# Kernel tuning notes

Hardware: AMD Instinct MI355X
Metric: run time of the kernel (lower is better)

The kernel has to match this reference:

```python
import jax, jax.numpy as jnp
import numpy as np

D_MODEL, D_HEAD, N_HEAD, PERIOD = 1024, 64, 16, 30
B, T1, T2 = 2, 2048, 2048


def setup_inputs() -> dict:
    key = jax.random.key(0)
    ks = jax.random.split(key, 7)
    s_in = 1.0 / np.sqrt(D_MODEL)
    s_out = 1.0 / np.sqrt(N_HEAD * D_HEAD)
    return {
        "x": jax.random.normal(ks[0], (B, T1, D_MODEL), dtype=jnp.float32),
        "context": jax.random.normal(ks[1], (B, T2, D_MODEL), dtype=jnp.float32),
        "Wq": jax.random.uniform(ks[2], (N_HEAD * D_HEAD, D_MODEL), jnp.float32, -s_in, s_in),
        "Wk": jax.random.uniform(ks[3], (N_HEAD * D_HEAD, D_MODEL), jnp.float32, -s_in, s_in),
        "Wv": jax.random.uniform(ks[4], (N_HEAD * D_HEAD, D_MODEL), jnp.float32, -s_in, s_in),
        "Wo": jax.random.uniform(ks[5], (D_MODEL, N_HEAD * D_HEAD), jnp.float32, -s_out, s_out),
        "bo": jax.random.uniform(ks[6], (D_MODEL,), jnp.float32, -s_out, s_out),
    }


def reference(x, context, Wq, Wk, Wv, Wo, bo):
    Bx, T1x, _ = x.shape
    T2x = context.shape[1]
    scale = 1.0 / np.sqrt(D_HEAD).astype(np.float32)
    # projections (torch Linear: y = x @ W^T)
    q = (x @ Wq.T).reshape(Bx, T1x, N_HEAD, D_HEAD)
    k = (context @ Wk.T).reshape(Bx, T2x, N_HEAD, D_HEAD)
    v = (context @ Wv.T).reshape(Bx, T2x, N_HEAD, D_HEAD)
    # attention scores [B, H, T1, T2]
    scores = jnp.einsum('bihd,bjhd->bhij', q, k) * scale
    # ALiBi-style periodic distance bias
    dist = jnp.abs(jnp.arange(T1x)[:, None] - jnp.arange(T2x)[None, :])  # [T1,T2]
    bias = -(dist // PERIOD).astype(jnp.float32)                          # [T1,T2]
    head_scale = jnp.power(2.0, -jnp.arange(1, N_HEAD + 1, dtype=jnp.float32))
    biased = scores + bias[None, None, :, :] * head_scale[None, :, None, None]
    attn = jax.nn.softmax(biased, axis=-1)
    out = jnp.einsum('bhij,bjhd->bihd', attn, v).reshape(Bx, T1x, N_HEAD * D_HEAD)
    # output projection; dropout is identity in eval mode
    return out @ Wo.T + bo
```

## Files before the change

kernel.cpp:

```cpp
#include <hip/hip_runtime.h>
#include <hip/hip_fp16.h>

typedef _Float16 f16;
typedef __attribute__((ext_vector_type(8))) _Float16 f16x8;
typedef __attribute__((ext_vector_type(4))) _Float16 f16x4;
typedef __attribute__((ext_vector_type(2))) __fp16 fp16x2;
typedef __attribute__((ext_vector_type(4))) float f32x4;
typedef __attribute__((ext_vector_type(16))) float f32x16;

#define DM 1024
#define NH 16
#define DH 64
#define TT 2048
#define LOG2E 1.4426950408889634f
#define QSCALE 0.18033688f

__device__ __forceinline__ void gl16(const void* g, void* l) {
  __builtin_amdgcn_global_load_lds((const __attribute__((address_space(1))) void*)g,
                                   (__attribute__((address_space(3))) void*)l, 16, 0, 0);
}

__global__ __launch_bounds__(256) void cvt_all(const float* __restrict__ x, const float* __restrict__ cx,
                                               const float* __restrict__ wq, const float* __restrict__ wk,
                                               const float* __restrict__ wv, const float* __restrict__ wo,
                                               f16* __restrict__ xb, f16* __restrict__ cb,
                                               f16* __restrict__ wqb, f16* __restrict__ wkb,
                                               f16* __restrict__ wvb, f16* __restrict__ wob) {
  int idx = blockIdx.x * 256 + threadIdx.x;
  int stride = gridDim.x * 256;
  for (int i = idx; i < 3145728; i += stride) {
    const float* src; f16* dst; int off; float s = 1.0f;
    if (i < 2097152) {
      if (i < 1048576) { src = x; dst = xb; off = i; }
      else { src = cx; dst = cb; off = i - 1048576; }
    } else {
      int j = i - 2097152;
      int wsel = j >> 18;
      off = j & 262143;
      if (wsel == 0) { src = wq; dst = wqb; s = QSCALE; }
      else if (wsel == 1) { src = wk; dst = wkb; }
      else if (wsel == 2) { src = wv; dst = wvb; }
      else { src = wo; dst = wob; }
    }
    float4 v = reinterpret_cast<const float4*>(src)[off];
    f16x4 o = { (f16)(v.x * s), (f16)(v.y * s), (f16)(v.z * s), (f16)(v.w * s) };
    reinterpret_cast<f16x4*>(dst)[off] = o;
  }
}

__global__ __launch_bounds__(256) void fbgen(f16* __restrict__ FB) {
  int i = blockIdx.x;
  int j0 = threadIdx.x * 8;
  f16x8 v;
#pragma unroll
  for (int e = 0; e < 8; e++) {
    int d = i - (j0 + e); d = (d < 0) ? -d : d;
    v[e] = (f16)(d / 30);
  }
  *reinterpret_cast<f16x8*>(&FB[(size_t)i * TT + j0]) = v;
}

__device__ __forceinline__ void gemm_mainloop(const f16* __restrict__ A, const f16* __restrict__ W,
                                              int bm, int bn, f16 (*As)[4096], f16 (*Bs)[4096],
                                              f32x4 (&acc)[4][4]) {
  int t = threadIdx.x;
  int w = t >> 6;
  int lane = t & 63, lr = lane & 15, g = lane >> 4;
  int wr = w >> 1, wc = w & 1;
  int scol = ((t & 3) ^ ((t >> 3) & 3)) * 8;
  const f16* a0 = A + (size_t)(bm + (t >> 2)) * DM + scol;
  const f16* b0 = W + (size_t)(bn + (t >> 2)) * DM + scol;
  int wo = w * 512;
  int szg = ((lr >> 1) & 3) << 4;

  auto STG = [&](int bufi, int kt) {
    gl16(a0 + kt, As[bufi] + wo);
    gl16(a0 + kt + (size_t)64 * DM, As[bufi] + 2048 + wo);
    gl16(b0 + kt, Bs[bufi] + wo);
    gl16(b0 + kt + (size_t)64 * DM, Bs[bufi] + 2048 + wo);
  };

  STG(0, 0);
  __syncthreads();
  int buf = 0;
  for (int kt = 0; kt < DM; kt += 32) {
    if (kt + 32 < DM) STG(buf ^ 1, kt + 32);
    const char* Ab = (const char*)As[buf];
    const char* Bb = (const char*)Bs[buf];
    f16x8 af[4], bf[4];
#pragma unroll
    for (int mi = 0; mi < 4; mi++) {
      int row = wr * 64 + mi * 16 + lr;
      af[mi] = *reinterpret_cast<const f16x8*>(Ab + row * 64 + ((g << 4) ^ szg));
    }
#pragma unroll
    for (int ni = 0; ni < 4; ni++) {
      int row = wc * 64 + ni * 16 + lr;
      bf[ni] = *reinterpret_cast<const f16x8*>(Bb + row * 64 + ((g << 4) ^ szg));
    }
    __builtin_amdgcn_s_setprio(1);
#pragma unroll
    for (int mi = 0; mi < 4; mi++)
#pragma unroll
      for (int ni = 0; ni < 4; ni++)
        acc[mi][ni] = __builtin_amdgcn_mfma_f32_16x16x32_f16(af[mi], bf[ni], acc[mi][ni], 0, 0, 0);
    __builtin_amdgcn_s_setprio(0);
    __syncthreads();
    buf ^= 1;
  }
}

__global__ __launch_bounds__(256) void qkv_gemm(const f16* __restrict__ xb, const f16* __restrict__ cb,
                                                const f16* __restrict__ wq, const f16* __restrict__ wk,
                                                const f16* __restrict__ wv,
                                                f16* __restrict__ Qo, f16* __restrict__ Ko,
                                                f16* __restrict__ Vt) {
  __shared__ f16 As[2][4096];
  __shared__ f16 Bs[2][4096];
  int gid = blockIdx.x >> 8;
  int bid = blockIdx.x & 255;
  int bm = (bid >> 3) * 128, bn = (bid & 7) * 128;
  const f16* A = (gid == 0) ? xb : cb;
  const f16* W = (gid == 0) ? wq : ((gid == 1) ? wk : wv);
  f32x4 acc[4][4] = {};
  gemm_mainloop(A, W, bm, bn, As, Bs, acc);

  int t = threadIdx.x, w = t >> 6, lane = t & 63, lr = lane & 15, g = lane >> 4;
  int wr = w >> 1, wc = w & 1;
  if (gid < 2) {
    f16* out = (gid == 0) ? Qo : Ko;
#pragma unroll
    for (int mi = 0; mi < 4; mi++) {
      int m0 = bm + wr * 64 + mi * 16 + 4 * g;
      int b = m0 >> 11, i0 = m0 & 2047;
#pragma unroll
      for (int ni = 0; ni < 4; ni++) {
        int n = bn + wc * 64 + ni * 16 + lr;
        int h = n >> 6, d = n & 63;
        size_t base = (((size_t)(b * NH + h)) * TT + i0) * DH + d;
#pragma unroll
        for (int r = 0; r < 4; r++)
          out[base + (size_t)r * DH] = (f16)acc[mi][ni][r];
      }
    }
  } else {
#pragma unroll
    for (int mi = 0; mi < 4; mi++) {
      int m0 = bm + wr * 64 + mi * 16 + 4 * g;
      int b = m0 >> 11, j0 = m0 & 2047;
#pragma unroll
      for (int ni = 0; ni < 4; ni++) {
        int n = bn + wc * 64 + ni * 16 + lr;
        int h = n >> 6, d = n & 63;
        f16x4 pk = { (f16)acc[mi][ni][0], (f16)acc[mi][ni][1],
                     (f16)acc[mi][ni][2], (f16)acc[mi][ni][3] };
        *reinterpret_cast<f16x4*>(&Vt[(((size_t)(b * NH + h)) * DH + d) * TT + j0]) = pk;
      }
    }
  }
}

__global__ __launch_bounds__(256) void out_gemm(const f16* __restrict__ Ob, const f16* __restrict__ wo,
                                                const float* __restrict__ bo, float* __restrict__ Y) {
  __shared__ f16 As[2][4096];
  __shared__ f16 Bs[2][4096];
  int bid = blockIdx.x;
  int bm = (bid >> 3) * 128, bn = (bid & 7) * 128;
  f32x4 acc[4][4] = {};
  gemm_mainloop(Ob, wo, bm, bn, As, Bs, acc);
  int t = threadIdx.x, w = t >> 6, lane = t & 63, lr = lane & 15, g = lane >> 4;
  int wr = w >> 1, wc = w & 1;
#pragma unroll
  for (int mi = 0; mi < 4; mi++) {
    int m0 = bm + wr * 64 + mi * 16 + 4 * g;
#pragma unroll
    for (int ni = 0; ni < 4; ni++) {
      int n = bn + wc * 64 + ni * 16 + lr;
      float bias = bo[n];
#pragma unroll
      for (int r = 0; r < 4; r++)
        Y[(size_t)(m0 + r) * DM + n] = acc[mi][ni][r] + bias;
    }
  }
}

__global__ __launch_bounds__(256, 2) void attn_kernel(const f16* __restrict__ Q, const f16* __restrict__ K,
                                                      const f16* __restrict__ V, const f16* __restrict__ FB,
                                                      f16* __restrict__ O) {
  __shared__ f16 KV[2][8192];
  int o = blockIdx.x;
  int x = o & 7, idx = o >> 3;
  int bh = 4 * x + (idx >> 4), qt = idx & 15;
  int h = bh & 15, b = bh >> 4;
  int t = threadIdx.x, w = t >> 6, lane = t & 63;
  int col = lane & 31, hi = lane >> 5;
  int qi = qt * 128 + w * 32 + col;

  const f16* qp = Q + ((size_t)bh * TT + qi) * DH + hi * 8;
  f16x8 qf[4];
  qf[0] = *reinterpret_cast<const f16x8*>(qp);
  qf[1] = *reinterpret_cast<const f16x8*>(qp + 16);
  qf[2] = *reinterpret_cast<const f16x8*>(qp + 32);
  qf[3] = *reinterpret_cast<const f16x8*>(qp + 48);

  const float nc2 = -exp2f(-(float)(h + 1)) * LOG2E;
  const f16* fbrow = FB + (size_t)qi * TT + hi * 8;

  float lsum = 0.f;
  f32x16 oacc[2] = {};

  int trow = t >> 3;
  int graw = (t & 7) ^ (trow & 7);
  int j0 = 16 * ((t >> 7) & 1) + 8 * ((t >> 5) & 1) + 4 * ((t >> 6) & 1) + ((t >> 3) & 3);
  const f16* ksrc = K + ((size_t)bh * TT + j0) * DH + graw * 8;
  const f16* vsrc = V + ((size_t)bh * DH + trow) * TT + graw * 8;
  int wo = w * 512;

  auto STG = [&](int bufi, int kv0) {
    f16* base = KV[bufi];
    gl16(ksrc + (size_t)kv0 * DH, base + wo);
    gl16(ksrc + (size_t)(kv0 + 32) * DH, base + 2048 + wo);
    gl16(vsrc + kv0, base + 4096 + wo);
    gl16(vsrc + (size_t)32 * TT + kv0, base + 6144 + wo);
  };

  int rbase = col * 128;
  int gsw[4];
#pragma unroll
  for (int s = 0; s < 4; s++) gsw[s] = (((2 * s + hi) ^ (lane & 7)) << 4);

  STG(0, 0);
  __syncthreads();
  int buf = 0;

  for (int kv0 = 0; kv0 < TT; kv0 += 64) {
    if (kv0 + 64 < TT) STG(buf ^ 1, kv0 + 64);
    f16x8 fbv[4];
    fbv[0] = *reinterpret_cast<const f16x8*>(fbrow + kv0);
    fbv[1] = *reinterpret_cast<const f16x8*>(fbrow + kv0 + 16);
    fbv[2] = *reinterpret_cast<const f16x8*>(fbrow + kv0 + 32);
    fbv[3] = *reinterpret_cast<const f16x8*>(fbrow + kv0 + 48);

    const char* Kb = (const char*)KV[buf];
    const char* Vb = Kb + 8192;

    f32x16 sj[2] = {};
    __builtin_amdgcn_s_setprio(1);
#pragma unroll
    for (int s = 0; s < 4; s++) {
      f16x8 ka = *reinterpret_cast<const f16x8*>(Kb + rbase + gsw[s]);
      f16x8 kb = *reinterpret_cast<const f16x8*>(Kb + 4096 + rbase + gsw[s]);
      sj[0] = __builtin_amdgcn_mfma_f32_32x32x16_f16(ka, qf[s], sj[0], 0, 0, 0);
      sj[1] = __builtin_amdgcn_mfma_f32_32x32x16_f16(kb, qf[s], sj[1], 0, 0, 0);
    }
    __builtin_amdgcn_s_setprio(0);

    f16x8 pb[4];
#pragma unroll
    for (int s = 0; s < 4; s++) {
      const int jb = s >> 1, ro = 8 * (s & 1);
      float p[8];
#pragma unroll
      for (int e = 0; e < 8; e++) {
        float sx = fmaf((float)fbv[s][e], nc2, sj[jb][ro + e]);
        p[e] = __builtin_amdgcn_exp2f(sx);
      }
      lsum += ((p[0] + p[1]) + (p[2] + p[3])) + ((p[4] + p[5]) + (p[6] + p[7]));
      union { f16x8 v; fp16x2 hh[4]; } pu;
      pu.hh[0] = __builtin_amdgcn_cvt_pkrtz(p[0], p[1]);
      pu.hh[1] = __builtin_amdgcn_cvt_pkrtz(p[2], p[3]);
      pu.hh[2] = __builtin_amdgcn_cvt_pkrtz(p[4], p[5]);
      pu.hh[3] = __builtin_amdgcn_cvt_pkrtz(p[6], p[7]);
      pb[s] = pu.v;
    }

    __builtin_amdgcn_s_setprio(1);
#pragma unroll
    for (int s = 0; s < 4; s++) {
      f16x8 va0 = *reinterpret_cast<const f16x8*>(Vb + rbase + gsw[s]);
      f16x8 va1 = *reinterpret_cast<const f16x8*>(Vb + 4096 + rbase + gsw[s]);
      oacc[0] = __builtin_amdgcn_mfma_f32_32x32x16_f16(va0, pb[s], oacc[0], 0, 0, 0);
      oacc[1] = __builtin_amdgcn_mfma_f32_32x32x16_f16(va1, pb[s], oacc[1], 0, 0, 0);
    }
    __builtin_amdgcn_s_setprio(0);
    __syncthreads();
    buf ^= 1;
  }

  lsum += __shfl_xor(lsum, 32, 64);
  float inv = __builtin_amdgcn_rcpf(lsum);

  size_t ob = ((size_t)b * TT + qi) * DM + h * DH + 4 * hi;
#pragma unroll
  for (int db = 0; db < 2; db++)
#pragma unroll
    for (int k = 0; k < 4; k++) {
      f16x4 o4 = { (f16)(oacc[db][4 * k] * inv),     (f16)(oacc[db][4 * k + 1] * inv),
                   (f16)(oacc[db][4 * k + 2] * inv), (f16)(oacc[db][4 * k + 3] * inv) };
      *reinterpret_cast<f16x4*>(&O[ob + 32 * db + 8 * k]) = o4;
    }
}

extern "C" void kernel_launch(void* const* d_in, const int* in_sizes, int n_in,
                              void* d_out, int out_size, void* d_ws, size_t ws_size,
                              hipStream_t stream) {
  const float* x  = (const float*)d_in[0];
  const float* cx = (const float*)d_in[1];
  const float* Wq = (const float*)d_in[2];
  const float* Wk = (const float*)d_in[3];
  const float* Wv = (const float*)d_in[4];
  const float* Wo = (const float*)d_in[5];
  const float* bo = (const float*)d_in[6];
  float* Y = (float*)d_out;

  const size_t NTOK = (size_t)2 * TT;
  f16* p = (f16*)d_ws;
  f16* xb  = p; p += NTOK * DM;
  f16* cb  = p; p += NTOK * DM;
  f16* wqb = p; p += (size_t)DM * DM;
  f16* wkb = p; p += (size_t)DM * DM;
  f16* wvb = p; p += (size_t)DM * DM;
  f16* wob = p; p += (size_t)DM * DM;
  f16* Qb  = p; p += NTOK * DM;
  f16* Kb  = p; p += NTOK * DM;
  f16* Vtb = p; p += NTOK * DM;
  f16* Ob  = p; p += NTOK * DM;
  f16* FBt = xb;

  cvt_all<<<2048, 256, 0, stream>>>(x, cx, Wq, Wk, Wv, Wo, xb, cb, wqb, wkb, wvb, wob);
  qkv_gemm<<<768, 256, 0, stream>>>(xb, cb, wqb, wkb, wvb, Qb, Kb, Vtb);
  fbgen<<<TT, 256, 0, stream>>>(FBt);
  attn_kernel<<<512, 256, 0, stream>>>(Qb, Kb, Vtb, FBt, Ob);
  out_gemm<<<256, 256, 0, stream>>>(Ob, wob, bo, Y);
}
```

Baseline: 132.7 us.

## Halve attention block size to two waves and double grid

Result: slower. 135.6 us (+2.2%).

```diff
diff --git a/kernel.cpp b/kernel.cpp
--- a/kernel.cpp
+++ b/kernel.cpp
@@ -184,17 +184,17 @@
   }
 }
 
-__global__ __launch_bounds__(256, 2) void attn_kernel(const f16* __restrict__ Q, const f16* __restrict__ K,
+__global__ __launch_bounds__(128, 2) void attn_kernel(const f16* __restrict__ Q, const f16* __restrict__ K,
                                                       const f16* __restrict__ V, const f16* __restrict__ FB,
                                                       f16* __restrict__ O) {
   __shared__ f16 KV[2][8192];
   int o = blockIdx.x;
   int x = o & 7, idx = o >> 3;
-  int bh = 4 * x + (idx >> 4), qt = idx & 15;
+  int bh = 4 * x + (idx >> 5), qt = idx & 31;
   int h = bh & 15, b = bh >> 4;
   int t = threadIdx.x, w = t >> 6, lane = t & 63;
   int col = lane & 31, hi = lane >> 5;
-  int qi = qt * 128 + w * 32 + col;
+  int qi = qt * 64 + w * 32 + col;
 
   const f16* qp = Q + ((size_t)bh * TT + qi) * DH + hi * 8;
   f16x8 qf[4];
@@ -206,28 +206,35 @@
   const float nc2 = -exp2f(-(float)(h + 1)) * LOG2E;
   const f16* fbrow = FB + (size_t)qi * TT + hi * 8;
 
-  float lsum = 0.f;
+  f32x4 rsv = { 0.f, 0.f, 0.f, 0.f };
   f32x16 oacc[2] = {};
 
-  int trow = t >> 3;
-  int graw = (t & 7) ^ (trow & 7);
-  int j0 = 16 * ((t >> 7) & 1) + 8 * ((t >> 5) & 1) + 4 * ((t >> 6) & 1) + ((t >> 3) & 3);
-  const f16* ksrc = K + ((size_t)bh * TT + j0) * DH + graw * 8;
-  const f16* vsrc = V + ((size_t)bh * DH + trow) * TT + graw * 8;
-  int wo = w * 512;
-
-  auto STG = [&](int bufi, int kv0) {
-    f16* base = KV[bufi];
-    gl16(ksrc + (size_t)kv0 * DH, base + wo);
-    gl16(ksrc + (size_t)(kv0 + 32) * DH, base + 2048 + wo);
-    gl16(vsrc + kv0, base + 4096 + wo);
-    gl16(vsrc + (size_t)32 * TT + kv0, base + 6144 + wo);
+  int r = lane >> 3, gcol = lane & 7;
+  const f16 *kp[4], *vp[4];
+#pragma unroll
+  for (int c = 0; c < 4; c++) {
+    int dg = gcol ^ r ^ (3 * (c >> 1));
+    int J = 32 * w + 16 * (c >> 1) + 8 * (r >> 2) + 4 * (c & 1) + (r & 3);
+    kp[c] = K + ((size_t)bh * TT + J) * DH + dg * 8;
+    int dv = 32 * w + 8 * c + r;
+    vp[c] = V + ((size_t)bh * DH + dv) * TT + dg * 8;
+  }
+  f16* ldsK = KV[0] + w * 2048;
+
+  auto STG = [&](int bufi, int kvo) {
+    f16* base = KV[bufi] + w * 2048;
+#pragma unroll
+    for (int c = 0; c < 4; c++) {
+      gl16(kp[c] + (size_t)kvo * DH, base + c * 512);
+      gl16(vp[c] + kvo, base + 4096 + c * 512);
+    }
   };
 
   int rbase = col * 128;
+  int fr = (lane & 7) ^ (3 * ((lane >> 4) & 1));
   int gsw[4];
 #pragma unroll
-  for (int s = 0; s < 4; s++) gsw[s] = (((2 * s + hi) ^ (lane & 7)) << 4);
+  for (int s = 0; s < 4; s++) gsw[s] = ((2 * s + hi) ^ fr) << 4;
 
   STG(0, 0);
   __syncthreads();
@@ -265,7 +272,9 @@
         float sx = fmaf((float)fbv[s][e], nc2, sj[jb][ro + e]);
         p[e] = __builtin_amdgcn_exp2f(sx);
       }
-      lsum += ((p[0] + p[1]) + (p[2] + p[3])) + ((p[4] + p[5]) + (p[6] + p[7]));
+      f32x4 pl = { p[0], p[1], p[2], p[3] };
+      f32x4 ph = { p[4], p[5], p[6], p[7] };
+      rsv += pl + ph;
       union { f16x8 v; fp16x2 hh[4]; } pu;
       pu.hh[0] = __builtin_amdgcn_cvt_pkrtz(p[0], p[1]);
       pu.hh[1] = __builtin_amdgcn_cvt_pkrtz(p[2], p[3]);
@@ -287,6 +296,7 @@
     buf ^= 1;
   }
 
+  float lsum = (rsv[0] + rsv[1]) + (rsv[2] + rsv[3]);
   lsum += __shfl_xor(lsum, 32, 64);
   float inv = __builtin_amdgcn_rcpf(lsum);
 
@@ -330,6 +340,6 @@
   cvt_all<<<2048, 256, 0, stream>>>(x, cx, Wq, Wk, Wv, Wo, xb, cb, wqb, wkb, wvb, wob);
   qkv_gemm<<<768, 256, 0, stream>>>(xb, cb, wqb, wkb, wvb, Qb, Kb, Vtb);
   fbgen<<<TT, 256, 0, stream>>>(FBt);
-  attn_kernel<<<512, 256, 0, stream>>>(Qb, Kb, Vtb, FBt, Ob);
+  attn_kernel<<<1024, 128, 0, stream>>>(Qb, Kb, Vtb, FBt, Ob);
   out_gemm<<<256, 256, 0, stream>>>(Ob, wob, bo, Y);
 }
```
